# Kernel tuning notes

Hardware: AMD Instinct MI355X
Metric: run time of the kernel (lower is better)

Reference implementation:

```python
import jax, jax.numpy as jnp
import numpy as np

B, N, D, H = 2, 2048, 1024, 16
HD = D // H  # head dim = 64
SCALING = (D / H) ** 0.5  # sqrt(64) = 8
EPS = 1e-5


def setup_inputs() -> dict:
    key = jax.random.key(0)
    k1, k2, k3 = jax.random.split(key, 3)
    return {
        "z": jax.random.normal(k1, (B, N, D), dtype=jnp.float32),
        "ln_scale": jnp.ones((D,), dtype=jnp.float32),
        "ln_bias": jnp.zeros((D,), dtype=jnp.float32),
        "w_qkv": jax.random.normal(k2, (D, 3 * D), dtype=jnp.float32) * (D ** -0.5),
        "w_proj": jax.random.normal(k3, (D, D), dtype=jnp.float32) * (D ** -0.5),
        "b_proj": jnp.zeros((D,), dtype=jnp.float32),
    }


def reference(z, ln_scale, ln_bias, w_qkv, w_proj, b_proj):
    b, n, d = z.shape
    # LayerNorm (pre-norm)
    mu = jnp.mean(z, axis=-1, keepdims=True)
    var = jnp.mean(jnp.square(z - mu), axis=-1, keepdims=True)
    zn = (z - mu) / jnp.sqrt(var + EPS) * ln_scale + ln_bias
    # QKV projection: [b, n, 3D]
    qkv = zn @ w_qkv
    # einops 'b n (h d qkv_n) -> qkv_n b h n d': qkv index is innermost
    qkv5 = qkv.reshape(b, n, H, HD, 3)  # [b, n, h, d, 3]
    q = jnp.transpose(qkv5[..., 0], (0, 2, 1, 3))  # [b, h, n, d]
    k = jnp.transpose(qkv5[..., 1], (0, 2, 1, 3))
    v = jnp.transpose(qkv5[..., 2], (0, 2, 1, 3))
    # Attention: scores scaled AFTER the matmul, as in the source
    scores = jnp.einsum('bhqd,bhkd->bhqk', q, k) / SCALING
    att = jax.nn.softmax(scores, axis=-1)
    out = jnp.einsum('bhal,bhlv->bhav', att, v)  # [b, h, n, d]
    out = jnp.transpose(out, (0, 2, 1, 3)).reshape(b, n, d)  # merge heads
    out = out @ w_proj + b_proj  # projection (dropout p=0)
    return z + out
```

## Files before the change

kernel.cpp:

```cpp
#include <hip/hip_runtime.h>
#include <stdint.h>
#include <math.h>

typedef unsigned short u16;
typedef float f32x4 __attribute__((ext_vector_type(4)));
typedef __bf16 bf16x8 __attribute__((ext_vector_type(8)));

__device__ __forceinline__ u16 f2bf(float f) {
    union { float f; uint32_t u; } c; c.f = f;
    return (u16)((c.u + 0x7FFFu + ((c.u >> 16) & 1u)) >> 16);
}

__device__ __forceinline__ void gload_lds16(const void* g, void* l) {
    __builtin_amdgcn_global_load_lds(
        (const __attribute__((address_space(1))) unsigned int*)g,
        (__attribute__((address_space(3))) unsigned int*)l, 16, 0, 0);
}

__global__ __launch_bounds__(256) void prep_kernel(const float* __restrict__ z,
                                                   const float* __restrict__ sc,
                                                   const float* __restrict__ bs,
                                                   const float* __restrict__ w_qkv,
                                                   const float* __restrict__ w_proj,
                                                   u16* __restrict__ zn,
                                                   u16* __restrict__ wqkvT,
                                                   u16* __restrict__ wprojT) {
    __shared__ __align__(16) float t[32][68];
    const int tid = threadIdx.x;
    const int bid = blockIdx.x;

    if (bid < 4096) {
        float* red = &t[0][0];
        const int row = bid;
        const float4 v = ((const float4*)(z + (size_t)row * 1024))[tid];
        float s = v.x + v.y + v.z + v.w;
        #pragma unroll
        for (int off = 32; off > 0; off >>= 1) s += __shfl_xor(s, off);
        if ((tid & 63) == 0) red[tid >> 6] = s;
        __syncthreads();
        const float mean = (red[0] + red[1] + red[2] + red[3]) * (1.0f / 1024.0f);
        const float dx = v.x - mean, dy = v.y - mean, dz = v.z - mean, dw = v.w - mean;
        float q = dx * dx + dy * dy + dz * dz + dw * dw;
        #pragma unroll
        for (int off = 32; off > 0; off >>= 1) q += __shfl_xor(q, off);
        if ((tid & 63) == 0) red[4 + (tid >> 6)] = q;
        __syncthreads();
        const float var = (red[4] + red[5] + red[6] + red[7]) * (1.0f / 1024.0f);
        const float rstd = rsqrtf(var + 1e-5f);
        const float4 scv = ((const float4*)sc)[tid];
        const float4 bsv = ((const float4*)bs)[tid];
        const u16 o0 = f2bf(dx * rstd * scv.x + bsv.x);
        const u16 o1 = f2bf(dy * rstd * scv.y + bsv.y);
        const u16 o2 = f2bf(dz * rstd * scv.z + bsv.z);
        const u16 o3 = f2bf(dw * rstd * scv.w + bsv.w);
        uint2 pk;
        pk.x = (uint32_t)o0 | ((uint32_t)o1 << 16);
        pk.y = (uint32_t)o2 | ((uint32_t)o3 << 16);
        *(uint2*)&zn[(size_t)row * 1024 + tid * 4] = pk;
        return;
    }

    const float* in;
    u16* out;
    int N, permute, bx, by;
    if (bid < 4096 + 1536) {
        const int r = bid - 4096;
        in = w_qkv; out = wqkvT; N = 3072; permute = 1;
        bx = r % 48; by = r / 48;
    } else {
        const int r = bid - 4096 - 1536;
        in = w_proj; out = wprojT; N = 1024; permute = 0;
        bx = r % 16; by = r / 16;
    }
    const int kb = by * 32, nb = bx * 64;
    const int lr = tid >> 3, lq = tid & 7;
    const float* src = &in[(size_t)(kb + lr) * N + nb + lq * 8];
    const float4 va = *(const float4*)src;
    const float4 vb = *(const float4*)(src + 4);
    *(float4*)&t[lr][lq * 8] = va;
    *(float4*)&t[lr][lq * 8 + 4] = vb;
    __syncthreads();
    const int cj = tid >> 6, c = tid & 63;
    const int col = nb + c;
    int np = col;
    if (permute) {
        const int h = col / 192, rem = col - h * 192;
        const int d = rem / 3, s = rem - d * 3;
        np = s * 1024 + h * 64 + d;
    }
    u16 pk[8];
    #pragma unroll
    for (int u = 0; u < 8; ++u) pk[u] = f2bf(t[cj * 8 + u][c]);
    *(uint4*)&out[(size_t)np * 1024 + kb + cj * 8] = *(const uint4*)pk;
}

__global__ __launch_bounds__(256, 3) void gemm_qkv(const u16* __restrict__ A,
                                                   const u16* __restrict__ Bt,
                                                   u16* __restrict__ qbuf,
                                                   u16* __restrict__ kbuf,
                                                   u16* __restrict__ vT) {
    __shared__ __align__(16) u16 sm[64 * 136];
    u16* const As = sm;
    u16* const Bs = sm + 4096;
    const int tid = threadIdx.x;
    const int wave = tid >> 6, lane = tid & 63;
    const int quad = lane >> 4, l16 = lane & 15;
    const int wm = (wave >> 1) * 64, wn = (wave & 1) * 64;
    const int lin = blockIdx.y * 32 + blockIdx.x;
    const int nlin = (lin & 7) * 96 + (lin >> 3);
    const int bxs = nlin & 31, bys = nlin >> 5;
    const int row0 = bxs * 128, col0 = bys * 128;
    const int gr = lane >> 2, gc = (lane & 3) * 8;
    f32x4 acc[4][4] = {};
    for (int kt = 0; kt < 1024; kt += 32) {
        __syncthreads();
        #pragma unroll
        for (int i = 0; i < 2; ++i) {
            const int rb = wave * 16 + i * 64;
            gload_lds16(&A[(size_t)(row0 + rb + gr) * 1024 + kt + gc], &As[rb * 32]);
            gload_lds16(&Bt[(size_t)(col0 + rb + gr) * 1024 + kt + gc], &Bs[rb * 32]);
        }
        __syncthreads();
        bf16x8 ax[4], bx[4];
        #pragma unroll
        for (int t = 0; t < 4; ++t) {
            ax[t] = *(const bf16x8*)&As[(wm + t * 16 + l16) * 32 + quad * 8];
            bx[t] = *(const bf16x8*)&Bs[(wn + t * 16 + l16) * 32 + quad * 8];
        }
        #pragma unroll
        for (int mt = 0; mt < 4; ++mt)
            #pragma unroll
            for (int nt = 0; nt < 4; ++nt)
                acc[mt][nt] = __builtin_amdgcn_mfma_f32_16x16x32_bf16(ax[mt], bx[nt], acc[mt][nt], 0, 0, 0);
    }
    const int s = col0 >> 10;
    if (s < 2) {
        u16* const dst = (s == 0) ? qbuf : kbuf;
        const float scl = (s == 0) ? 0.125f * 1.44269504088896f : 1.0f;
        #pragma unroll
        for (int mt = 0; mt < 4; ++mt) {
            #pragma unroll
            for (int nt = 0; nt < 4; ++nt) {
                #pragma unroll
                for (int e = 0; e < 4; ++e) {
                    const int row = row0 + wm + mt * 16 + quad * 4 + e;
                    const int col = col0 + wn + nt * 16 + l16;
                    const int b = row >> 11, n = row & 2047;
                    const int h = (col >> 6) & 15, d = col & 63;
                    dst[((size_t)(b * 16 + h) * 2048 + n) * 64 + d] = f2bf(acc[mt][nt][e] * scl);
                }
            }
        }
    } else {
        const int b = row0 >> 11, n0 = row0 & 2047;
        const int h0 = (col0 >> 6) & 15;
        for (int hh = 0; hh < 2; ++hh) {
            __syncthreads();
            if ((wave & 1) == hh) {
                #pragma unroll
                for (int mt = 0; mt < 4; ++mt) {
                    const int rl = wm + mt * 16 + quad * 4;
                    #pragma unroll
                    for (int nt = 0; nt < 4; ++nt) {
                        const int cl = nt * 16 + l16;
                        u16 tmp[4];
                        #pragma unroll
                        for (int e = 0; e < 4; ++e) tmp[e] = f2bf(acc[mt][nt][e]);
                        *(uint2*)&sm[cl * 136 + rl] = *(const uint2*)tmp;
                    }
                }
            }
            __syncthreads();
            const int bh = b * 16 + h0 + hh;
            #pragma unroll
            for (int pass = 0; pass < 4; ++pass) {
                const int chunk = pass * 256 + tid;
                const int d = chunk >> 4;
                const int nc = chunk & 15;
                const uint4 vv = *(const uint4*)&sm[d * 136 + nc * 8];
                *(uint4*)&vT[((size_t)bh * 64 + d) * 2048 + n0 + nc * 8] = vv;
            }
        }
    }
}

__global__ __launch_bounds__(256, 2) void attn_kernel(const u16* __restrict__ qb,
                                                      const u16* __restrict__ kb,
                                                      const u16* __restrict__ vT,
                                                      u16* __restrict__ att_out) {
    __shared__ __align__(16) u16 smem[2][16384];
    const int tid = threadIdx.x;
    const int wave = tid >> 6, lane = tid & 63;
    const int quad = lane >> 4, l16 = lane & 15;
    const int lin = blockIdx.y * 16 + blockIdx.x;
    const int nlin = (lin & 7) * 64 + (lin >> 3);
    const int qt = nlin & 15, bh = nlin >> 4;
    const int b = bh >> 4, h = bh & 15;

    const u16* qrowA = &qb[(size_t)(bh * 2048 + qt * 128 + wave * 32 + l16) * 64];
    const bf16x8 qA0 = *(const bf16x8*)&qrowA[quad * 8];
    const bf16x8 qA1 = *(const bf16x8*)&qrowA[32 + quad * 8];
    const u16* qrowB = qrowA + 16 * 64;
    const bf16x8 qB0 = *(const bf16x8*)&qrowB[quad * 8];
    const bf16x8 qB1 = *(const bf16x8*)&qrowB[32 + quad * 8];

    const u16* ksrc[4];
    const u16* vsrc[4];
    int kofs[4], vofs[4];
    #pragma unroll
    for (int j = 0; j < 4; ++j) {
        const int p = 8 * wave + 32 * j + (lane >> 3);
        const int kr = (p & 0x60) | ((p & 12) << 1) | ((p & 16) >> 2) | (p & 3);
        const int gk = (lane & 7) ^ (p & 7);
        ksrc[j] = kb + ((size_t)bh * 2048 + kr) * 64 + gk * 8;
        kofs[j] = (8 * wave + 32 * j) * 64;
        const int d = 4 * wave + 16 * j + (lane >> 4);
        const int gv = (lane & 15) ^ (d & 15);
        vsrc[j] = vT + ((size_t)bh * 64 + d) * 2048 + gv * 8;
        vofs[j] = 8192 + (4 * wave + 16 * j) * 128;
    }

    f32x4 oA[4] = {}, oB[4] = {};
    f32x4 lA = {}, lB = {};
    bf16x8 ones;
    #pragma unroll
    for (int i = 0; i < 8; ++i) ones[i] = (__bf16)1.0f;

    #pragma unroll
    for (int j = 0; j < 4; ++j) {
        gload_lds16(ksrc[j], &smem[0][kofs[j]]);
        gload_lds16(vsrc[j], &smem[0][vofs[j]]);
        ksrc[j] += 128 * 64;
        vsrc[j] += 128;
    }

    for (int kt = 0; kt < 16; ++kt) {
        __syncthreads();
        if (kt < 15) {
            u16* nb_ = smem[(kt + 1) & 1];
            #pragma unroll
            for (int j = 0; j < 4; ++j) {
                gload_lds16(ksrc[j], &nb_[kofs[j]]);
                gload_lds16(vsrc[j], &nb_[vofs[j]]);
                ksrc[j] += 128 * 64;
                vsrc[j] += 128;
            }
        }
        const u16* Ks = smem[kt & 1];
        const u16* Vs = smem[kt & 1] + 8192;

        f32x4 sA[8] = {}, sB[8] = {};
        __builtin_amdgcn_s_setprio(1);
        #pragma unroll
        for (int nt = 0; nt < 8; ++nt) {
            const int r = nt * 16 + l16;
            const bf16x8 k0 = *(const bf16x8*)&Ks[r * 64 + (((quad) ^ (r & 7)) << 3)];
            const bf16x8 k1 = *(const bf16x8*)&Ks[r * 64 + (((quad + 4) ^ (r & 7)) << 3)];
            sA[nt] = __builtin_amdgcn_mfma_f32_16x16x32_bf16(k0, qA0, sA[nt], 0, 0, 0);
            sA[nt] = __builtin_amdgcn_mfma_f32_16x16x32_bf16(k1, qA1, sA[nt], 0, 0, 0);
            sB[nt] = __builtin_amdgcn_mfma_f32_16x16x32_bf16(k0, qB0, sB[nt], 0, 0, 0);
            sB[nt] = __builtin_amdgcn_mfma_f32_16x16x32_bf16(k1, qB1, sB[nt], 0, 0, 0);
        }
        __builtin_amdgcn_s_setprio(0);

        bf16x8 apA[4], apB[4];
        #pragma unroll
        for (int nt = 0; nt < 8; ++nt) {
            #pragma unroll
            for (int e = 0; e < 4; ++e) {
                apA[nt >> 1][(nt & 1) * 4 + e] = (__bf16)__builtin_amdgcn_exp2f(sA[nt][e]);
                apB[nt >> 1][(nt & 1) * 4 + e] = (__bf16)__builtin_amdgcn_exp2f(sB[nt][e]);
            }
        }

        __builtin_amdgcn_s_setprio(1);
        #pragma unroll
        for (int vt = 0; vt < 4; ++vt) {
            const int dd = vt * 16 + l16;
            #pragma unroll
            for (int c = 0; c < 4; ++c) {
                const bf16x8 vf = *(const bf16x8*)&Vs[dd * 128 + (((c * 4 + quad) ^ l16) << 3)];
                oA[vt] = __builtin_amdgcn_mfma_f32_16x16x32_bf16(apA[c], vf, oA[vt], 0, 0, 0);
                oB[vt] = __builtin_amdgcn_mfma_f32_16x16x32_bf16(apB[c], vf, oB[vt], 0, 0, 0);
            }
        }
        #pragma unroll
        for (int c = 0; c < 4; ++c) {
            lA = __builtin_amdgcn_mfma_f32_16x16x32_bf16(apA[c], ones, lA, 0, 0, 0);
            lB = __builtin_amdgcn_mfma_f32_16x16x32_bf16(apB[c], ones, lB, 0, 0, 0);
        }
        __builtin_amdgcn_s_setprio(0);
    }

    #pragma unroll
    for (int e = 0; e < 4; ++e) {
        const float invA = 1.0f / lA[e];
        const float invB = 1.0f / lB[e];
        const int nA = qt * 128 + wave * 32 + quad * 4 + e;
        #pragma unroll
        for (int vt = 0; vt < 4; ++vt) {
            att_out[(size_t)(b * 2048 + nA) * 1024 + h * 64 + vt * 16 + l16] = f2bf(oA[vt][e] * invA);
            att_out[(size_t)(b * 2048 + nA + 16) * 1024 + h * 64 + vt * 16 + l16] = f2bf(oB[vt][e] * invB);
        }
    }
}

__global__ __launch_bounds__(256, 3) void gemm_proj(const u16* __restrict__ A,
                                                    const u16* __restrict__ Bt,
                                                    const float* __restrict__ bias,
                                                    const float* __restrict__ z,
                                                    float* __restrict__ out) {
    __shared__ __align__(16) u16 sm[2 * 4096];
    u16* const As = sm;
    u16* const Bs = sm + 4096;
    const int tid = threadIdx.x;
    const int wave = tid >> 6, lane = tid & 63;
    const int quad = lane >> 4, l16 = lane & 15;
    const int wm = (wave >> 1) * 64, wn = (wave & 1) * 64;
    const int lin = blockIdx.y * 32 + blockIdx.x;
    const int nlin = (lin & 7) * 32 + (lin >> 3);
    const int bxs = nlin & 31, bys = nlin >> 5;
    const int row0 = bxs * 128, col0 = bys * 128;
    const int gr = lane >> 2, gc = (lane & 3) * 8;
    f32x4 acc[4][4] = {};
    for (int kt = 0; kt < 1024; kt += 32) {
        __syncthreads();
        #pragma unroll
        for (int i = 0; i < 2; ++i) {
            const int rb = wave * 16 + i * 64;
            gload_lds16(&A[(size_t)(row0 + rb + gr) * 1024 + kt + gc], &As[rb * 32]);
            gload_lds16(&Bt[(size_t)(col0 + rb + gr) * 1024 + kt + gc], &Bs[rb * 32]);
        }
        __syncthreads();
        bf16x8 ax[4], bx[4];
        #pragma unroll
        for (int t = 0; t < 4; ++t) {
            ax[t] = *(const bf16x8*)&As[(wm + t * 16 + l16) * 32 + quad * 8];
            bx[t] = *(const bf16x8*)&Bs[(wn + t * 16 + l16) * 32 + quad * 8];
        }
        #pragma unroll
        for (int mt = 0; mt < 4; ++mt)
            #pragma unroll
            for (int nt = 0; nt < 4; ++nt)
                acc[mt][nt] = __builtin_amdgcn_mfma_f32_16x16x32_bf16(ax[mt], bx[nt], acc[mt][nt], 0, 0, 0);
    }
    #pragma unroll
    for (int mt = 0; mt < 4; ++mt) {
        #pragma unroll
        for (int nt = 0; nt < 4; ++nt) {
            #pragma unroll
            for (int e = 0; e < 4; ++e) {
                const int row = row0 + wm + mt * 16 + quad * 4 + e;
                const int col = col0 + wn + nt * 16 + l16;
                out[(size_t)row * 1024 + col] = acc[mt][nt][e] + bias[col] + z[(size_t)row * 1024 + col];
            }
        }
    }
}

extern "C" void kernel_launch(void* const* d_in, const int* in_sizes, int n_in,
                              void* d_out, int out_size, void* d_ws, size_t ws_size,
                              hipStream_t stream) {
    const float* z        = (const float*)d_in[0];
    const float* ln_scale = (const float*)d_in[1];
    const float* ln_bias  = (const float*)d_in[2];
    const float* w_qkv    = (const float*)d_in[3];
    const float* w_proj   = (const float*)d_in[4];
    const float* b_proj   = (const float*)d_in[5];
    float* out = (float*)d_out;

    char* ws = (char*)d_ws;
    u16* zn     = (u16*)(ws);
    u16* wqkvT  = (u16*)(ws + (8u << 20));
    u16* wprojT = (u16*)(ws + (14u << 20));
    u16* qbuf   = (u16*)(ws + (16u << 20));
    u16* kbuf   = (u16*)(ws + (24u << 20));
    u16* vT     = (u16*)(ws + (32u << 20));
    u16* att_o  = (u16*)(ws + (40u << 20));

    prep_kernel<<<dim3(4096 + 1536 + 512), 256, 0, stream>>>(
        z, ln_scale, ln_bias, w_qkv, w_proj, zn, wqkvT, wprojT);
    gemm_qkv<<<dim3(32, 24), 256, 0, stream>>>(zn, wqkvT, qbuf, kbuf, vT);
    attn_kernel<<<dim3(16, 32), 256, 0, stream>>>(qbuf, kbuf, vT, att_o);
    gemm_proj<<<dim3(32, 8), 256, 0, stream>>>(att_o, wprojT, b_proj, z, out);
}
```

Measured before the change: 177.3 us.

## Halve attention query and key tiles to double grid size and occupancy

Shrinks the attention block from 128 to 64 query rows (one 16-row group per wave instead of two) and the K/V tile from 128 to 64 keys. The LDS double buffer halves, the V swizzle is redone for 64-wide rows, and launch bounds rise to 4 blocks per CU with a 1024-block grid. The aim is more parallelism and latency hiding on the many CUs. In exchange each K/V tile is reused by half as many query rows, doubling K/V traffic from global memory and LDS, and there are twice as many barrier iterations.

```diff
diff --git a/kernel.cpp b/kernel.cpp
--- a/kernel.cpp
+++ b/kernel.cpp
@@ -184,124 +184,110 @@
     }
 }
 
-__global__ __launch_bounds__(256, 2) void attn_kernel(const u16* __restrict__ qb,
+__global__ __launch_bounds__(256, 4) void attn_kernel(const u16* __restrict__ qb,
                                                       const u16* __restrict__ kb,
                                                       const u16* __restrict__ vT,
                                                       u16* __restrict__ att_out) {
-    __shared__ __align__(16) u16 smem[2][16384];
+    __shared__ __align__(16) u16 smem[2][8192];
     const int tid = threadIdx.x;
     const int wave = tid >> 6, lane = tid & 63;
     const int quad = lane >> 4, l16 = lane & 15;
-    const int lin = blockIdx.y * 16 + blockIdx.x;
-    const int nlin = (lin & 7) * 64 + (lin >> 3);
-    const int qt = nlin & 15, bh = nlin >> 4;
+    const int lin = blockIdx.y * 32 + blockIdx.x;
+    const int nlin = (lin & 7) * 128 + (lin >> 3);
+    const int qt = nlin & 31, bh = nlin >> 5;
     const int b = bh >> 4, h = bh & 15;
 
-    const u16* qrowA = &qb[(size_t)(bh * 2048 + qt * 128 + wave * 32 + l16) * 64];
-    const bf16x8 qA0 = *(const bf16x8*)&qrowA[quad * 8];
-    const bf16x8 qA1 = *(const bf16x8*)&qrowA[32 + quad * 8];
-    const u16* qrowB = qrowA + 16 * 64;
-    const bf16x8 qB0 = *(const bf16x8*)&qrowB[quad * 8];
-    const bf16x8 qB1 = *(const bf16x8*)&qrowB[32 + quad * 8];
-
-    const u16* ksrc[4];
-    const u16* vsrc[4];
-    int kofs[4], vofs[4];
-    #pragma unroll
-    for (int j = 0; j < 4; ++j) {
+    const u16* qrow = &qb[(size_t)(bh * 2048 + qt * 64 + wave * 16 + l16) * 64];
+    const bf16x8 qA0 = *(const bf16x8*)&qrow[quad * 8];
+    const bf16x8 qA1 = *(const bf16x8*)&qrow[32 + quad * 8];
+
+    const u16* ksrc[2];
+    const u16* vsrc[2];
+    int kofs[2], vofs[2];
+    #pragma unroll
+    for (int j = 0; j < 2; ++j) {
         const int p = 8 * wave + 32 * j + (lane >> 3);
         const int kr = (p & 0x60) | ((p & 12) << 1) | ((p & 16) >> 2) | (p & 3);
         const int gk = (lane & 7) ^ (p & 7);
         ksrc[j] = kb + ((size_t)bh * 2048 + kr) * 64 + gk * 8;
         kofs[j] = (8 * wave + 32 * j) * 64;
-        const int d = 4 * wave + 16 * j + (lane >> 4);
-        const int gv = (lane & 15) ^ (d & 15);
+        const int d = 8 * wave + 32 * j + (lane >> 3);
+        const int gv = (lane & 7) ^ ((d >> 1) & 7);
         vsrc[j] = vT + ((size_t)bh * 64 + d) * 2048 + gv * 8;
-        vofs[j] = 8192 + (4 * wave + 16 * j) * 128;
-    }
-
-    f32x4 oA[4] = {}, oB[4] = {};
-    f32x4 lA = {}, lB = {};
+        vofs[j] = 4096 + (8 * wave + 32 * j) * 64;
+    }
+
+    f32x4 oA[4] = {};
+    f32x4 lA = {};
     bf16x8 ones;
     #pragma unroll
     for (int i = 0; i < 8; ++i) ones[i] = (__bf16)1.0f;
 
     #pragma unroll
-    for (int j = 0; j < 4; ++j) {
+    for (int j = 0; j < 2; ++j) {
         gload_lds16(ksrc[j], &smem[0][kofs[j]]);
         gload_lds16(vsrc[j], &smem[0][vofs[j]]);
-        ksrc[j] += 128 * 64;
-        vsrc[j] += 128;
-    }
-
-    for (int kt = 0; kt < 16; ++kt) {
-        __syncthreads();
-        if (kt < 15) {
+        ksrc[j] += 64 * 64;
+        vsrc[j] += 64;
+    }
+
+    for (int kt = 0; kt < 32; ++kt) {
+        __syncthreads();
+        if (kt < 31) {
             u16* nb_ = smem[(kt + 1) & 1];
             #pragma unroll
-            for (int j = 0; j < 4; ++j) {
+            for (int j = 0; j < 2; ++j) {
                 gload_lds16(ksrc[j], &nb_[kofs[j]]);
                 gload_lds16(vsrc[j], &nb_[vofs[j]]);
-                ksrc[j] += 128 * 64;
-                vsrc[j] += 128;
+                ksrc[j] += 64 * 64;
+                vsrc[j] += 64;
             }
         }
         const u16* Ks = smem[kt & 1];
-        const u16* Vs = smem[kt & 1] + 8192;
-
-        f32x4 sA[8] = {}, sB[8] = {};
+        const u16* Vs = smem[kt & 1] + 4096;
+
+        f32x4 sA[4] = {};
         __builtin_amdgcn_s_setprio(1);
         #pragma unroll
-        for (int nt = 0; nt < 8; ++nt) {
+        for (int nt = 0; nt < 4; ++nt) {
             const int r = nt * 16 + l16;
             const bf16x8 k0 = *(const bf16x8*)&Ks[r * 64 + (((quad) ^ (r & 7)) << 3)];
             const bf16x8 k1 = *(const bf16x8*)&Ks[r * 64 + (((quad + 4) ^ (r & 7)) << 3)];
             sA[nt] = __builtin_amdgcn_mfma_f32_16x16x32_bf16(k0, qA0, sA[nt], 0, 0, 0);
             sA[nt] = __builtin_amdgcn_mfma_f32_16x16x32_bf16(k1, qA1, sA[nt], 0, 0, 0);
-            sB[nt] = __builtin_amdgcn_mfma_f32_16x16x32_bf16(k0, qB0, sB[nt], 0, 0, 0);
-            sB[nt] = __builtin_amdgcn_mfma_f32_16x16x32_bf16(k1, qB1, sB[nt], 0, 0, 0);
         }
         __builtin_amdgcn_s_setprio(0);
 
-        bf16x8 apA[4], apB[4];
-        #pragma unroll
-        for (int nt = 0; nt < 8; ++nt) {
-            #pragma unroll
-            for (int e = 0; e < 4; ++e) {
-                apA[nt >> 1][(nt & 1) * 4 + e] = (__bf16)__builtin_amdgcn_exp2f(sA[nt][e]);
-                apB[nt >> 1][(nt & 1) * 4 + e] = (__bf16)__builtin_amdgcn_exp2f(sB[nt][e]);
-            }
-        }
+        bf16x8 ap[2];
+        #pragma unroll
+        for (int nt = 0; nt < 4; ++nt)
+            #pragma unroll
+            for (int e = 0; e < 4; ++e)
+                ap[nt >> 1][(nt & 1) * 4 + e] = (__bf16)__builtin_amdgcn_exp2f(sA[nt][e]);
 
         __builtin_amdgcn_s_setprio(1);
         #pragma unroll
         for (int vt = 0; vt < 4; ++vt) {
             const int dd = vt * 16 + l16;
             #pragma unroll
-            for (int c = 0; c < 4; ++c) {
-                const bf16x8 vf = *(const bf16x8*)&Vs[dd * 128 + (((c * 4 + quad) ^ l16) << 3)];
-                oA[vt] = __builtin_amdgcn_mfma_f32_16x16x32_bf16(apA[c], vf, oA[vt], 0, 0, 0);
-                oB[vt] = __builtin_amdgcn_mfma_f32_16x16x32_bf16(apB[c], vf, oB[vt], 0, 0, 0);
-            }
-        }
-        #pragma unroll
-        for (int c = 0; c < 4; ++c) {
-            lA = __builtin_amdgcn_mfma_f32_16x16x32_bf16(apA[c], ones, lA, 0, 0, 0);
-            lB = __builtin_amdgcn_mfma_f32_16x16x32_bf16(apB[c], ones, lB, 0, 0, 0);
-        }
+            for (int c = 0; c < 2; ++c) {
+                const bf16x8 vf = *(const bf16x8*)&Vs[dd * 64 + (((c * 4 + quad) ^ ((dd >> 1) & 7)) << 3)];
+                oA[vt] = __builtin_amdgcn_mfma_f32_16x16x32_bf16(ap[c], vf, oA[vt], 0, 0, 0);
+            }
+        }
+        #pragma unroll
+        for (int c = 0; c < 2; ++c)
+            lA = __builtin_amdgcn_mfma_f32_16x16x32_bf16(ap[c], ones, lA, 0, 0, 0);
         __builtin_amdgcn_s_setprio(0);
     }
 
     #pragma unroll
     for (int e = 0; e < 4; ++e) {
         const float invA = 1.0f / lA[e];
-        const float invB = 1.0f / lB[e];
-        const int nA = qt * 128 + wave * 32 + quad * 4 + e;
-        #pragma unroll
-        for (int vt = 0; vt < 4; ++vt) {
+        const int nA = qt * 64 + wave * 16 + quad * 4 + e;
+        #pragma unroll
+        for (int vt = 0; vt < 4; ++vt)
             att_out[(size_t)(b * 2048 + nA) * 1024 + h * 64 + vt * 16 + l16] = f2bf(oA[vt][e] * invA);
-            att_out[(size_t)(b * 2048 + nA + 16) * 1024 + h * 64 + vt * 16 + l16] = f2bf(oB[vt][e] * invB);
-        }
     }
 }
 
@@ -381,6 +367,6 @@
     prep_kernel<<<dim3(4096 + 1536 + 512), 256, 0, stream>>>(
         z, ln_scale, ln_bias, w_qkv, w_proj, zn, wqkvT, wprojT);
     gemm_qkv<<<dim3(32, 24), 256, 0, stream>>>(zn, wqkvT, qbuf, kbuf, vT);
-    attn_kernel<<<dim3(16, 32), 256, 0, stream>>>(qbuf, kbuf, vT, att_o);
+    attn_kernel<<<dim3(32, 32), 256, 0, stream>>>(qbuf, kbuf, vT, att_o);
     gemm_proj<<<dim3(32, 8), 256, 0, stream>>>(att_o, wprojT, b_proj, z, out);
 }
```

After: 182.6 us. 1.03x slower.

## Software-pipeline attention with 64-key tiles, triple-buffered LDS, and QK/PV overlap

Applied to the files above, without the earlier changes.

The attention kernel now uses 64-key tiles instead of 128 and a three-slot LDS ring buffer. The main loop is software-pipelined so each iteration issues the QK^T MFMAs for the current tile alongside the exp and PV MFMAs for the previous tile, hiding exp latency behind independent matrix work. The V tile layout and XOR swizzle change to match the 64-wide tiles. The trade-offs are twice as many barriers, more live score registers, and a more complex prologue and epilogue, which could hurt occupancy at two blocks per CU.

```diff
diff --git a/kernel.cpp b/kernel.cpp
--- a/kernel.cpp
+++ b/kernel.cpp
@@ -188,7 +188,7 @@
                                                       const u16* __restrict__ kb,
                                                       const u16* __restrict__ vT,
                                                       u16* __restrict__ att_out) {
-    __shared__ __align__(16) u16 smem[2][16384];
+    __shared__ __align__(16) u16 smem[3 * 8192];
     const int tid = threadIdx.x;
     const int wave = tid >> 6, lane = tid & 63;
     const int quad = lane >> 4, l16 = lane & 15;
@@ -204,93 +204,111 @@
     const bf16x8 qB0 = *(const bf16x8*)&qrowB[quad * 8];
     const bf16x8 qB1 = *(const bf16x8*)&qrowB[32 + quad * 8];
 
-    const u16* ksrc[4];
-    const u16* vsrc[4];
-    int kofs[4], vofs[4];
+    const u16* ksrc[2];
+    const u16* vsrc[2];
+    int kofs[2], vofs[2];
     #pragma unroll
-    for (int j = 0; j < 4; ++j) {
+    for (int j = 0; j < 2; ++j) {
         const int p = 8 * wave + 32 * j + (lane >> 3);
         const int kr = (p & 0x60) | ((p & 12) << 1) | ((p & 16) >> 2) | (p & 3);
         const int gk = (lane & 7) ^ (p & 7);
         ksrc[j] = kb + ((size_t)bh * 2048 + kr) * 64 + gk * 8;
         kofs[j] = (8 * wave + 32 * j) * 64;
-        const int d = 4 * wave + 16 * j + (lane >> 4);
-        const int gv = (lane & 15) ^ (d & 15);
+        const int d = 8 * wave + 32 * j + (lane >> 3);
+        const int gv = (lane & 7) ^ ((d >> 1) & 7);
         vsrc[j] = vT + ((size_t)bh * 64 + d) * 2048 + gv * 8;
-        vofs[j] = 8192 + (4 * wave + 16 * j) * 128;
+        vofs[j] = 4096 + (8 * wave + 32 * j) * 64;
     }
 
     f32x4 oA[4] = {}, oB[4] = {};
     f32x4 lA = {}, lB = {};
+    f32x4 s0A[4], s0B[4], s1A[4], s1B[4];
     bf16x8 ones;
     #pragma unroll
     for (int i = 0; i < 8; ++i) ones[i] = (__bf16)1.0f;
 
-    #pragma unroll
-    for (int j = 0; j < 4; ++j) {
-        gload_lds16(ksrc[j], &smem[0][kofs[j]]);
-        gload_lds16(vsrc[j], &smem[0][vofs[j]]);
-        ksrc[j] += 128 * 64;
-        vsrc[j] += 128;
-    }
-
-    for (int kt = 0; kt < 16; ++kt) {
-        __syncthreads();
-        if (kt < 15) {
-            u16* nb_ = smem[(kt + 1) & 1];
-            #pragma unroll
-            for (int j = 0; j < 4; ++j) {
-                gload_lds16(ksrc[j], &nb_[kofs[j]]);
-                gload_lds16(vsrc[j], &nb_[vofs[j]]);
-                ksrc[j] += 128 * 64;
-                vsrc[j] += 128;
-            }
-        }
-        const u16* Ks = smem[kt & 1];
-        const u16* Vs = smem[kt & 1] + 8192;
-
-        f32x4 sA[8] = {}, sB[8] = {};
-        __builtin_amdgcn_s_setprio(1);
-        #pragma unroll
-        for (int nt = 0; nt < 8; ++nt) {
+    auto stage = [&](int buf) {
+        u16* dst = smem + buf * 8192;
+        #pragma unroll
+        for (int j = 0; j < 2; ++j) {
+            gload_lds16(ksrc[j], dst + kofs[j]);
+            gload_lds16(vsrc[j], dst + vofs[j]);
+            ksrc[j] += 64 * 64;
+            vsrc[j] += 64;
+        }
+    };
+    auto QK = [&](int buf, f32x4 (&sA)[4], f32x4 (&sB)[4]) {
+        const u16* Ks = smem + buf * 8192;
+        #pragma unroll
+        for (int nt = 0; nt < 4; ++nt) {
             const int r = nt * 16 + l16;
             const bf16x8 k0 = *(const bf16x8*)&Ks[r * 64 + (((quad) ^ (r & 7)) << 3)];
             const bf16x8 k1 = *(const bf16x8*)&Ks[r * 64 + (((quad + 4) ^ (r & 7)) << 3)];
-            sA[nt] = __builtin_amdgcn_mfma_f32_16x16x32_bf16(k0, qA0, sA[nt], 0, 0, 0);
-            sA[nt] = __builtin_amdgcn_mfma_f32_16x16x32_bf16(k1, qA1, sA[nt], 0, 0, 0);
-            sB[nt] = __builtin_amdgcn_mfma_f32_16x16x32_bf16(k0, qB0, sB[nt], 0, 0, 0);
-            sB[nt] = __builtin_amdgcn_mfma_f32_16x16x32_bf16(k1, qB1, sB[nt], 0, 0, 0);
-        }
-        __builtin_amdgcn_s_setprio(0);
-
-        bf16x8 apA[4], apB[4];
-        #pragma unroll
-        for (int nt = 0; nt < 8; ++nt) {
+            f32x4 a = {}, c = {};
+            a = __builtin_amdgcn_mfma_f32_16x16x32_bf16(k0, qA0, a, 0, 0, 0);
+            a = __builtin_amdgcn_mfma_f32_16x16x32_bf16(k1, qA1, a, 0, 0, 0);
+            c = __builtin_amdgcn_mfma_f32_16x16x32_bf16(k0, qB0, c, 0, 0, 0);
+            c = __builtin_amdgcn_mfma_f32_16x16x32_bf16(k1, qB1, c, 0, 0, 0);
+            sA[nt] = a;
+            sB[nt] = c;
+        }
+    };
+    auto EXPPV = [&](int buf, f32x4 (&sA)[4], f32x4 (&sB)[4]) {
+        bf16x8 apA[2], apB[2];
+        #pragma unroll
+        for (int nt = 0; nt < 4; ++nt)
             #pragma unroll
             for (int e = 0; e < 4; ++e) {
                 apA[nt >> 1][(nt & 1) * 4 + e] = (__bf16)__builtin_amdgcn_exp2f(sA[nt][e]);
                 apB[nt >> 1][(nt & 1) * 4 + e] = (__bf16)__builtin_amdgcn_exp2f(sB[nt][e]);
             }
-        }
-
-        __builtin_amdgcn_s_setprio(1);
+        const u16* Vs = smem + buf * 8192 + 4096;
         #pragma unroll
         for (int vt = 0; vt < 4; ++vt) {
             const int dd = vt * 16 + l16;
             #pragma unroll
-            for (int c = 0; c < 4; ++c) {
-                const bf16x8 vf = *(const bf16x8*)&Vs[dd * 128 + (((c * 4 + quad) ^ l16) << 3)];
+            for (int c = 0; c < 2; ++c) {
+                const bf16x8 vf = *(const bf16x8*)&Vs[dd * 64 + (((c * 4 + quad) ^ ((dd >> 1) & 7)) << 3)];
                 oA[vt] = __builtin_amdgcn_mfma_f32_16x16x32_bf16(apA[c], vf, oA[vt], 0, 0, 0);
                 oB[vt] = __builtin_amdgcn_mfma_f32_16x16x32_bf16(apB[c], vf, oB[vt], 0, 0, 0);
             }
         }
         #pragma unroll
-        for (int c = 0; c < 4; ++c) {
+        for (int c = 0; c < 2; ++c) {
             lA = __builtin_amdgcn_mfma_f32_16x16x32_bf16(apA[c], ones, lA, 0, 0, 0);
             lB = __builtin_amdgcn_mfma_f32_16x16x32_bf16(apB[c], ones, lB, 0, 0, 0);
         }
+    };
+
+    stage(0);
+    stage(1);
+    __syncthreads();
+    QK(0, s0A, s0B);
+
+    int bPrev = 0, bCur = 1, bNext = 2;
+    #pragma unroll 1
+    for (int tp = 0; tp < 15; ++tp) {
+        __syncthreads();
+        stage(bNext);
+        __builtin_amdgcn_s_setprio(1);
+        QK(bCur, s1A, s1B);
+        EXPPV(bPrev, s0A, s0B);
         __builtin_amdgcn_s_setprio(0);
-    }
+        bPrev = bCur; bCur = bNext; bNext = (bNext == 2) ? 0 : bNext + 1;
+        __syncthreads();
+        stage(bNext);
+        __builtin_amdgcn_s_setprio(1);
+        QK(bCur, s0A, s0B);
+        EXPPV(bPrev, s1A, s1B);
+        __builtin_amdgcn_s_setprio(0);
+        bPrev = bCur; bCur = bNext; bNext = (bNext == 2) ? 0 : bNext + 1;
+    }
+    __syncthreads();
+    __builtin_amdgcn_s_setprio(1);
+    QK(bCur, s1A, s1B);
+    EXPPV(bPrev, s0A, s0B);
+    EXPPV(bCur, s1A, s1B);
+    __builtin_amdgcn_s_setprio(0);
 
     #pragma unroll
     for (int e = 0; e < 4; ++e) {
```

New measurement: 179.8 us. No clear change (+1.4%).
